# Kernel optimization log

Hardware: AMD Instinct MI355X
Metric: run time of the kernel (lower is better)

## Reference

```python
import jax, jax.numpy as jnp
import numpy as np

FEATURE_DIM = 128
HIDDEN_DIM = 64
MAPPING_SIZE = 64
SCALE = 10.0
B, N, H, W = 8, 65536, 56, 56


def setup_inputs() -> dict:
    key = jax.random.key(0)
    ks = jax.random.split(key, 12)
    features = jax.random.normal(ks[0], (B, FEATURE_DIM, H, W), dtype=jnp.float32)
    # points in [-1, 1]^3
    points = jax.random.uniform(ks[1], (B, N, 3), dtype=jnp.float32, minval=-1.0, maxval=1.0)
    # realistic pinhole intrinsics for a 56x56 feature map
    k_mat = jnp.array([[56.0, 0.0, 28.0], [0.0, 56.0, 28.0], [0.0, 0.0, 1.0]], dtype=jnp.float32)
    k = jnp.broadcast_to(k_mat, (B, 3, 3))
    # extrinsics: identity rotation, translate z by 2 so points are in front of camera
    rt_mat = jnp.concatenate([jnp.eye(3, dtype=jnp.float32), jnp.array([[0.0], [0.0], [2.0]], dtype=jnp.float32)], axis=1)
    rt = jnp.broadcast_to(rt_mat, (B, 3, 4))
    # learned params
    B_gauss = jax.random.normal(ks[2], (MAPPING_SIZE, 3), dtype=jnp.float32) * SCALE
    input_dim = FEATURE_DIM + 2 * MAPPING_SIZE
    W1 = jax.random.normal(ks[3], (input_dim, HIDDEN_DIM), dtype=jnp.float32) * 0.05
    b1 = jnp.zeros((HIDDEN_DIM,), dtype=jnp.float32)
    W2 = jax.random.normal(ks[4], (HIDDEN_DIM, HIDDEN_DIM), dtype=jnp.float32) * 0.05
    b2 = jnp.zeros((HIDDEN_DIM,), dtype=jnp.float32)
    W3 = jax.random.normal(ks[5], (HIDDEN_DIM, HIDDEN_DIM), dtype=jnp.float32) * 0.05
    b3 = jnp.zeros((HIDDEN_DIM,), dtype=jnp.float32)
    W4 = jax.random.normal(ks[6], (HIDDEN_DIM, 1), dtype=jnp.float32) * 0.05
    b4 = jnp.zeros((1,), dtype=jnp.float32)
    return {"features": features, "points": points, "k": k, "rt": rt,
            "B_gauss": B_gauss, "W1": W1, "b1": b1, "W2": W2, "b2": b2,
            "W3": W3, "b3": b3, "W4": W4, "b4": b4}


def _grid_sample_bilinear_zeros(grid, x, y):
    # grid: (B, C, H, W); x, y: (B, N) pixel coords (align_corners=False already unnormalized)
    Bc, C, Hc, Wc = grid.shape
    g = jnp.transpose(grid, (0, 2, 3, 1))  # (B, H, W, C)
    x0 = jnp.floor(x)
    y0 = jnp.floor(y)
    wx1 = x - x0  # frac
    wy1 = y - y0
    wx0 = 1.0 - wx1
    wy0 = 1.0 - wy1
    x0i = x0.astype(jnp.int32)
    y0i = y0.astype(jnp.int32)
    bidx = jnp.arange(Bc, dtype=jnp.int32)[:, None]  # (B, 1)

    def gather(ix, iy):
        inb = ((ix >= 0) & (ix < Wc) & (iy >= 0) & (iy < Hc)).astype(grid.dtype)  # (B, N)
        vals = g[bidx, jnp.clip(iy, 0, Hc - 1), jnp.clip(ix, 0, Wc - 1)]  # (B, N, C)
        return vals * inb[..., None]

    out = (gather(x0i, y0i) * (wx0 * wy0)[..., None]
           + gather(x0i + 1, y0i) * (wx1 * wy0)[..., None]
           + gather(x0i, y0i + 1) * (wx0 * wy1)[..., None]
           + gather(x0i + 1, y0i + 1) * (wx1 * wy1)[..., None])
    return out  # (B, N, C)


def reference(features, points, k, rt, B_gauss, W1, b1, W2, b2, W3, b3, W4, b4):
    Bc, Nc, _ = points.shape
    Hc, Wc = features.shape[-2:]
    # --- camera projection ---
    homo = jnp.concatenate([points, jnp.ones((Bc, Nc, 1), dtype=points.dtype)], axis=2)  # (B,N,4)
    cam = jnp.einsum('bij,bnj->bni', rt, homo)   # (B,N,3)
    img = jnp.einsum('bij,bnj->bni', k, cam)     # (B,N,3)
    z = img[:, :, 2:3] + 1e-8
    uv = img[:, :, :2] / z
    valid = (img[:, :, 2:3] > 0).astype(points.dtype)  # (B,N,1)
    u_norm = (2.0 * uv[..., 0] + 1.0) / Wc - 1.0
    v_norm = (2.0 * uv[..., 1] + 1.0) / Hc - 1.0
    # grid_sample align_corners=False unnormalization: ix = ((g+1)*W - 1)/2
    x = ((u_norm + 1.0) * Wc - 1.0) * 0.5
    y = ((v_norm + 1.0) * Hc - 1.0) * 0.5
    img_feats = _grid_sample_bilinear_zeros(features, x, y) * valid  # (B,N,C)
    # --- Fourier mapping ---
    x_proj = (2.0 * np.pi) * jnp.einsum('bnd,md->bnm', points, B_gauss)  # (B,N,M)
    coord_feats = jnp.concatenate([jnp.sin(x_proj), jnp.cos(x_proj)], axis=-1)  # (B,N,2M)
    # --- MLP ---
    inp = jnp.concatenate([img_feats, coord_feats], axis=2)  # (B,N,C+2M)
    h = jax.nn.relu(inp @ W1 + b1)
    h = jax.nn.relu(h @ W2 + b2)
    h = jax.nn.relu(h @ W3 + b3)
    out = h @ W4 + b4  # (B,N,1)
    return out
```

## Files before the change

kernel.cpp:

```cpp
#include <hip/hip_runtime.h>

#define FDIM 128
#define HDIM 64
#define MSIZE 64
#define IMG_W 56
#define IMG_H 56
#define NPIX (IMG_W * IMG_H)
#define NB 8
#define NPTS 65536

typedef _Float16 f16x8 __attribute__((ext_vector_type(8)));
typedef float f32x4 __attribute__((ext_vector_type(4)));
typedef int i32x4 __attribute__((ext_vector_type(4)));

#define W2_OFF 16384
#define W3_OFF 20480
#define FT_BYTE_OFF 49152
#define TR_BLOCKS (NPIX / 64 * NB)

__device__ __forceinline__ void lds_fence() {
    __asm__ volatile("s_waitcnt lgkmcnt(0)" ::: "memory");
}

__global__ __launch_bounds__(256) void prep_kernel(const float* __restrict__ in,
                                                   const float* __restrict__ W1,
                                                   const float* __restrict__ W2,
                                                   const float* __restrict__ W3,
                                                   _Float16* __restrict__ ws) {
    if (blockIdx.x < TR_BLOCKS) {
        __shared__ float tile[64][129];
        _Float16* out = ws + FT_BYTE_OFF / 2;
        const int b = blockIdx.x / (NPIX / 64);
        const int pbase = (blockIdx.x % (NPIX / 64)) * 64;
        const int t = threadIdx.x;
        const float* src = in + (size_t)b * FDIM * NPIX;
        _Float16*    dst = out + (size_t)b * NPIX * FDIM;
        const int tx = t & 63;
        const int cg = t >> 6;
#pragma unroll
        for (int i = 0; i < 32; ++i) {
            int c = cg * 32 + i;
            tile[tx][c] = src[(size_t)c * NPIX + pbase + tx];
        }
        __syncthreads();
        const int sub = t >> 4;
        const int hk  = (t & 15) * 8;
#pragma unroll
        for (int g = 0; g < 4; ++g) {
            const int px = g * 16 + sub;
            f16x8 hv;
#pragma unroll
            for (int j = 0; j < 8; ++j) hv[j] = (_Float16)tile[px][hk + j];
            *(f16x8*)(dst + (size_t)(pbase + px) * FDIM + hk) = hv;
        }
    } else {
        const int t = (blockIdx.x - TR_BLOCKS) * 256 + threadIdx.x;
        const int l = t & 63;
        const int q = l >> 4;
        const int col = l & 15;
        const int frag = t >> 6;
        if (frag < 32) {
            const int kt = frag >> 2, nt = frag & 3;
#pragma unroll
            for (int j = 0; j < 8; ++j) {
                int k = kt * 32 + q * 8 + j;
                int row = (k < 128) ? k : (128 + (k & 1) * 64 + ((k - 128) >> 1));
                ws[((size_t)(frag * 64 + l)) * 8 + j] = (_Float16)W1[row * HDIM + nt * 16 + col];
            }
        } else if (frag < 40) {
            const int f2 = frag - 32;
            const int kt = f2 >> 2, nt = f2 & 3;
#pragma unroll
            for (int j = 0; j < 8; ++j) {
                int row = kt * 32 + q * 8 + j;
                ws[W2_OFF + ((size_t)(f2 * 64 + l)) * 8 + j] = (_Float16)W2[row * HDIM + nt * 16 + col];
            }
        } else {
            const int f3 = frag - 40;
            const int kt = f3 >> 2, nt = f3 & 3;
#pragma unroll
            for (int j = 0; j < 8; ++j) {
                int row = kt * 32 + q * 8 + j;
                ws[W3_OFF + ((size_t)(f3 * 64 + l)) * 8 + j] = (_Float16)W3[row * HDIM + nt * 16 + col];
            }
        }
    }
}

__global__ __launch_bounds__(256, 2) void decoder_mfma2(
    const _Float16* __restrict__ ft,
    const float* __restrict__ points,
    const float* __restrict__ Kmat, const float* __restrict__ Rt,
    const float* __restrict__ Bg,
    const _Float16* __restrict__ wfrag,
    const float* __restrict__ b1, const float* __restrict__ b2,
    const float* __restrict__ b3,
    const float* __restrict__ W4, const float* __restrict__ b4,
    float* __restrict__ out) {
    __shared__ _Float16 lds[4 * 64 * 72];
    const int tid = threadIdx.x;
    const int wid = tid >> 6;
    const int l   = tid & 63;
    const int q   = l >> 4;
    const int col = l & 15;
    const int b    = blockIdx.x & 7;
    const int grp  = blockIdx.x >> 3;
    const int base = b * NPTS + grp * 256 + wid * 64;
    const int gid  = base + l;
    _Float16* Ah = lds + wid * 64 * 72;
    float* sh = (float*)Ah;
    int*   shi = (int*)Ah;

    const float px = points[(size_t)gid * 3 + 0];
    const float py = points[(size_t)gid * 3 + 1];
    const float pz = points[(size_t)gid * 3 + 2];
    const float* rt = Rt + b * 12;
    const float* km = Kmat + b * 9;
    float cx = rt[0] * px + rt[1] * py + rt[2]  * pz + rt[3];
    float cy = rt[4] * px + rt[5] * py + rt[6]  * pz + rt[7];
    float cz = rt[8] * px + rt[9] * py + rt[10] * pz + rt[11];
    float ix = km[0] * cx + km[1] * cy + km[2] * cz;
    float iy = km[3] * cx + km[4] * cy + km[5] * cz;
    float iz = km[6] * cx + km[7] * cy + km[8] * cz;
    float z  = iz + 1e-8f;
    float u  = ix / z;
    float v  = iy / z;
    float valid = (iz > 0.0f) ? 1.0f : 0.0f;
    float u_norm = (2.0f * u + 1.0f) / (float)IMG_W - 1.0f;
    float v_norm = (2.0f * v + 1.0f) / (float)IMG_H - 1.0f;
    float x = ((u_norm + 1.0f) * (float)IMG_W - 1.0f) * 0.5f;
    float y = ((v_norm + 1.0f) * (float)IMG_H - 1.0f) * 0.5f;
    float x0f = floorf(x), y0f = floorf(y);
    float wx1 = x - x0f, wy1 = y - y0f;
    float wx0 = 1.0f - wx1, wy0 = 1.0f - wy1;
    int x0 = (int)x0f, y0 = (int)y0f;
    int x1 = x0 + 1, y1 = y0 + 1;
    int x0c = x0 < 0 ? 0 : (x0 > IMG_W - 1 ? IMG_W - 1 : x0);
    int x1c = x1 < 0 ? 0 : (x1 > IMG_W - 1 ? IMG_W - 1 : x1);
    int y0c = y0 < 0 ? 0 : (y0 > IMG_H - 1 ? IMG_H - 1 : y0);
    int y1c = y1 < 0 ? 0 : (y1 > IMG_H - 1 ? IMG_H - 1 : y1);
    float mx0 = (x0 >= 0 && x0 < IMG_W) ? 1.0f : 0.0f;
    float mx1 = (x1 >= 0 && x1 < IMG_W) ? 1.0f : 0.0f;
    float my0 = (y0 >= 0 && y0 < IMG_H) ? 1.0f : 0.0f;
    float my1 = (y1 >= 0 && y1 < IMG_H) ? 1.0f : 0.0f;
    const int pb = b * NPIX;
    sh[l * 12 + 0] = wx0 * wy0 * mx0 * my0 * valid;
    sh[l * 12 + 1] = wx1 * wy0 * mx1 * my0 * valid;
    sh[l * 12 + 2] = wx0 * wy1 * mx0 * my1 * valid;
    sh[l * 12 + 3] = wx1 * wy1 * mx1 * my1 * valid;
    shi[l * 12 + 4] = (pb + y0c * IMG_W + x0c) * FDIM;
    shi[l * 12 + 5] = (pb + y0c * IMG_W + x1c) * FDIM;
    shi[l * 12 + 6] = (pb + y1c * IMG_W + x0c) * FDIM;
    shi[l * 12 + 7] = (pb + y1c * IMG_W + x1c) * FDIM;
    sh[l * 12 + 8]  = px;
    sh[l * 12 + 9]  = py;
    sh[l * 12 + 10] = pz;
    lds_fence();

    const f32x4 zero4 = {0.0f, 0.0f, 0.0f, 0.0f};
    f32x4 acc[4][4];
#pragma unroll
    for (int mt = 0; mt < 4; ++mt)
#pragma unroll
        for (int nt = 0; nt < 4; ++nt) acc[mt][nt] = zero4;

    f32x4 wv[4];
    i32x4 iv[4];
    float qx[4], qy[4], qz[4];
#pragma unroll
    for (int mt = 0; mt < 4; ++mt) {
        const float* e = sh + (mt * 16 + col) * 12;
        wv[mt] = *(const f32x4*)(e);
        iv[mt] = *(const i32x4*)(e + 4);
        qx[mt] = e[8]; qy[mt] = e[9]; qz[mt] = e[10];
    }

#pragma unroll
    for (int ktf = 0; ktf < 4; ++ktf) {
        float bgx[4], bgy[4], bgz[4];
#pragma unroll
        for (int i = 0; i < 4; ++i) {
            const int m = ktf * 16 + q * 4 + i;
            bgx[i] = Bg[m * 3 + 0];
            bgy[i] = Bg[m * 3 + 1];
            bgz[i] = Bg[m * 3 + 2];
        }
        f16x8 bf[4];
#pragma unroll
        for (int nt = 0; nt < 4; ++nt)
            bf[nt] = *(const f16x8*)(wfrag + ((size_t)(((4 + ktf) * 4 + nt) * 64 + l)) * 8);
#pragma unroll
        for (int mt = 0; mt < 4; ++mt) {
            f16x8 af;
#pragma unroll
            for (int i = 0; i < 4; ++i) {
                float t = bgx[i] * qx[mt] + bgy[i] * qy[mt] + bgz[i] * qz[mt];
                float tf = t - floorf(t);
                af[2 * i]     = (_Float16)__builtin_amdgcn_sinf(tf);
                af[2 * i + 1] = (_Float16)__builtin_amdgcn_cosf(tf);
            }
#pragma unroll
            for (int nt = 0; nt < 4; ++nt)
                acc[mt][nt] = __builtin_amdgcn_mfma_f32_16x16x32_f16(af, bf[nt], acc[mt][nt], 0, 0, 0);
        }
    }

#pragma unroll
    for (int mt = 0; mt < 4; ++mt) {
        const _Float16 w0h = (_Float16)wv[mt].x, w1h = (_Float16)wv[mt].y;
        const _Float16 w2h = (_Float16)wv[mt].z, w3h = (_Float16)wv[mt].w;
        const int co0 = q * 8;
        f16x8 c00 = *(const f16x8*)(ft + iv[mt].x + co0);
        f16x8 c10 = *(const f16x8*)(ft + iv[mt].y + co0);
        f16x8 c01 = *(const f16x8*)(ft + iv[mt].z + co0);
        f16x8 c11 = *(const f16x8*)(ft + iv[mt].w + co0);
#pragma unroll
        for (int ktg = 0; ktg < 4; ++ktg) {
            f16x8 n00, n10, n01, n11;
            if (ktg < 3) {
                const int co = (ktg + 1) * 32 + q * 8;
                n00 = *(const f16x8*)(ft + iv[mt].x + co);
                n10 = *(const f16x8*)(ft + iv[mt].y + co);
                n01 = *(const f16x8*)(ft + iv[mt].z + co);
                n11 = *(const f16x8*)(ft + iv[mt].w + co);
            }
            f16x8 af = c00 * w0h + c10 * w1h + c01 * w2h + c11 * w3h;
#pragma unroll
            for (int nt = 0; nt < 4; ++nt) {
                f16x8 bf = *(const f16x8*)(wfrag + ((size_t)((ktg * 4 + nt) * 64 + l)) * 8);
                acc[mt][nt] = __builtin_amdgcn_mfma_f32_16x16x32_f16(af, bf, acc[mt][nt], 0, 0, 0);
            }
            c00 = n00; c10 = n10; c01 = n01; c11 = n11;
        }
    }

    float bb[4];
#pragma unroll
    for (int nt = 0; nt < 4; ++nt) bb[nt] = b1[nt * 16 + col];
#pragma unroll
    for (int mt = 0; mt < 4; ++mt)
#pragma unroll
        for (int nt = 0; nt < 4; ++nt)
#pragma unroll
            for (int r = 0; r < 4; ++r) {
                float hv = fmaxf(acc[mt][nt][r] + bb[nt], 0.0f);
                Ah[(mt * 16 + q * 4 + r) * 72 + nt * 16 + col] = (_Float16)hv;
            }
    lds_fence();

#pragma unroll
    for (int mt = 0; mt < 4; ++mt)
#pragma unroll
        for (int nt = 0; nt < 4; ++nt) acc[mt][nt] = zero4;
#pragma unroll
    for (int ktl = 0; ktl < 2; ++ktl) {
        f16x8 bf[4];
#pragma unroll
        for (int nt = 0; nt < 4; ++nt)
            bf[nt] = *(const f16x8*)(wfrag + W2_OFF + ((size_t)((ktl * 4 + nt) * 64 + l)) * 8);
#pragma unroll
        for (int mt = 0; mt < 4; ++mt) {
            f16x8 af = *(const f16x8*)(&Ah[(mt * 16 + col) * 72 + ktl * 32 + q * 8]);
#pragma unroll
            for (int nt = 0; nt < 4; ++nt)
                acc[mt][nt] = __builtin_amdgcn_mfma_f32_16x16x32_f16(af, bf[nt], acc[mt][nt], 0, 0, 0);
        }
    }
    lds_fence();
#pragma unroll
    for (int nt = 0; nt < 4; ++nt) bb[nt] = b2[nt * 16 + col];
#pragma unroll
    for (int mt = 0; mt < 4; ++mt)
#pragma unroll
        for (int nt = 0; nt < 4; ++nt)
#pragma unroll
            for (int r = 0; r < 4; ++r) {
                float hv = fmaxf(acc[mt][nt][r] + bb[nt], 0.0f);
                Ah[(mt * 16 + q * 4 + r) * 72 + nt * 16 + col] = (_Float16)hv;
            }
    lds_fence();

#pragma unroll
    for (int mt = 0; mt < 4; ++mt)
#pragma unroll
        for (int nt = 0; nt < 4; ++nt) acc[mt][nt] = zero4;
#pragma unroll
    for (int ktl = 0; ktl < 2; ++ktl) {
        f16x8 bf[4];
#pragma unroll
        for (int nt = 0; nt < 4; ++nt)
            bf[nt] = *(const f16x8*)(wfrag + W3_OFF + ((size_t)((ktl * 4 + nt) * 64 + l)) * 8);
#pragma unroll
        for (int mt = 0; mt < 4; ++mt) {
            f16x8 af = *(const f16x8*)(&Ah[(mt * 16 + col) * 72 + ktl * 32 + q * 8]);
#pragma unroll
            for (int nt = 0; nt < 4; ++nt)
                acc[mt][nt] = __builtin_amdgcn_mfma_f32_16x16x32_f16(af, bf[nt], acc[mt][nt], 0, 0, 0);
        }
    }

    float b3v[4], w4v[4];
#pragma unroll
    for (int nt = 0; nt < 4; ++nt) {
        b3v[nt] = b3[nt * 16 + col];
        w4v[nt] = W4[nt * 16 + col];
    }
    const float b4v = b4[0];
#pragma unroll
    for (int mt = 0; mt < 4; ++mt)
#pragma unroll
        for (int r = 0; r < 4; ++r) {
            float p = 0.0f;
#pragma unroll
            for (int nt = 0; nt < 4; ++nt)
                p = fmaf(fmaxf(acc[mt][nt][r] + b3v[nt], 0.0f), w4v[nt], p);
            p += __shfl_xor(p, 1);
            p += __shfl_xor(p, 2);
            p += __shfl_xor(p, 4);
            p += __shfl_xor(p, 8);
            if (col == 0) out[base + mt * 16 + q * 4 + r] = p + b4v;
        }
}

__global__ __launch_bounds__(64, 2) void decoder_valu(
    const float* __restrict__ feats, const float* __restrict__ points,
    const float* __restrict__ Kmat, const float* __restrict__ Rt,
    const float* __restrict__ Bg,
    const float* __restrict__ W1, const float* __restrict__ b1,
    const float* __restrict__ W2, const float* __restrict__ b2,
    const float* __restrict__ W3, const float* __restrict__ b3,
    const float* __restrict__ W4, const float* __restrict__ b4,
    float* __restrict__ out) {
    __shared__ float hbuf[64 * 65];
    const int tid = threadIdx.x;
    const int b   = blockIdx.x / (NPTS / 64);
    const int gid = blockIdx.x * 64 + tid;
    const float px = points[(size_t)gid * 3 + 0];
    const float py = points[(size_t)gid * 3 + 1];
    const float pz = points[(size_t)gid * 3 + 2];
    const float* rt = Rt + b * 12;
    const float* km = Kmat + b * 9;
    float cx = rt[0] * px + rt[1] * py + rt[2]  * pz + rt[3];
    float cy = rt[4] * px + rt[5] * py + rt[6]  * pz + rt[7];
    float cz = rt[8] * px + rt[9] * py + rt[10] * pz + rt[11];
    float ix = km[0] * cx + km[1] * cy + km[2] * cz;
    float iy = km[3] * cx + km[4] * cy + km[5] * cz;
    float iz = km[6] * cx + km[7] * cy + km[8] * cz;
    float z  = iz + 1e-8f;
    float u  = ix / z, v = iy / z;
    float valid = (iz > 0.0f) ? 1.0f : 0.0f;
    float u_norm = (2.0f * u + 1.0f) / (float)IMG_W - 1.0f;
    float v_norm = (2.0f * v + 1.0f) / (float)IMG_H - 1.0f;
    float x = ((u_norm + 1.0f) * (float)IMG_W - 1.0f) * 0.5f;
    float y = ((v_norm + 1.0f) * (float)IMG_H - 1.0f) * 0.5f;
    float x0f = floorf(x), y0f = floorf(y);
    float wx1 = x - x0f, wy1 = y - y0f;
    float wx0 = 1.0f - wx1, wy0 = 1.0f - wy1;
    int x0 = (int)x0f, y0 = (int)y0f;
    int x1 = x0 + 1, y1 = y0 + 1;
    int x0c = x0 < 0 ? 0 : (x0 > IMG_W - 1 ? IMG_W - 1 : x0);
    int x1c = x1 < 0 ? 0 : (x1 > IMG_W - 1 ? IMG_W - 1 : x1);
    int y0c = y0 < 0 ? 0 : (y0 > IMG_H - 1 ? IMG_H - 1 : y0);
    int y1c = y1 < 0 ? 0 : (y1 > IMG_H - 1 ? IMG_H - 1 : y1);
    float mx0 = (x0 >= 0 && x0 < IMG_W) ? 1.0f : 0.0f;
    float mx1 = (x1 >= 0 && x1 < IMG_W) ? 1.0f : 0.0f;
    float my0 = (y0 >= 0 && y0 < IMG_H) ? 1.0f : 0.0f;
    float my1 = (y1 >= 0 && y1 < IMG_H) ? 1.0f : 0.0f;
    float w00 = wx0 * wy0 * mx0 * my0 * valid;
    float w10 = wx1 * wy0 * mx1 * my0 * valid;
    float w01 = wx0 * wy1 * mx0 * my1 * valid;
    float w11 = wx1 * wy1 * mx1 * my1 * valid;
    float h[HDIM];
#pragma unroll
    for (int j = 0; j < HDIM; ++j) h[j] = b1[j];
    const float* fb = feats + (size_t)b * FDIM * NPIX;
    const int p00 = y0c * IMG_W + x0c, p10 = y0c * IMG_W + x1c;
    const int p01 = y1c * IMG_W + x0c, p11 = y1c * IMG_W + x1c;
#pragma unroll 1
    for (int c = 0; c < FDIM; ++c) {
        const float* fp = fb + (size_t)c * NPIX;
        float fv = w00 * fp[p00] + w10 * fp[p10] + w01 * fp[p01] + w11 * fp[p11];
        const float* wr = W1 + (size_t)c * HDIM;
#pragma unroll
        for (int j = 0; j < HDIM; ++j) h[j] = fmaf(fv, wr[j], h[j]);
    }
#pragma unroll 1
    for (int m = 0; m < MSIZE; ++m) {
        float t = Bg[m * 3 + 0] * px + Bg[m * 3 + 1] * py + Bg[m * 3 + 2] * pz;
        float tf = t - floorf(t);
        float s = __builtin_amdgcn_sinf(tf);
        float c = __builtin_amdgcn_cosf(tf);
        const float* wsn = W1 + (size_t)(FDIM + m) * HDIM;
        const float* wcs = W1 + (size_t)(FDIM + MSIZE + m) * HDIM;
#pragma unroll
        for (int j = 0; j < HDIM; ++j)
            h[j] = fmaf(s, wsn[j], fmaf(c, wcs[j], h[j]));
    }
    float* myh = &hbuf[tid * 65];
#pragma unroll
    for (int j = 0; j < HDIM; ++j) myh[j] = fmaxf(h[j], 0.0f);
    float h2[HDIM];
#pragma unroll
    for (int j = 0; j < HDIM; ++j) h2[j] = b2[j];
#pragma unroll 1
    for (int i = 0; i < HDIM; ++i) {
        float hi = myh[i];
        const float* wr = W2 + (size_t)i * HDIM;
#pragma unroll
        for (int j = 0; j < HDIM; ++j) h2[j] = fmaf(hi, wr[j], h2[j]);
    }
#pragma unroll
    for (int j = 0; j < HDIM; ++j) myh[j] = fmaxf(h2[j], 0.0f);
#pragma unroll
    for (int j = 0; j < HDIM; ++j) h[j] = b3[j];
#pragma unroll 1
    for (int i = 0; i < HDIM; ++i) {
        float hi = myh[i];
        const float* wr = W3 + (size_t)i * HDIM;
#pragma unroll
        for (int j = 0; j < HDIM; ++j) h[j] = fmaf(hi, wr[j], h[j]);
    }
    float acc = b4[0];
#pragma unroll
    for (int j = 0; j < HDIM; ++j) acc = fmaf(fmaxf(h[j], 0.0f), W4[j], acc);
    out[gid] = acc;
}

extern "C" void kernel_launch(void* const* d_in, const int* in_sizes, int n_in,
                              void* d_out, int out_size, void* d_ws, size_t ws_size,
                              hipStream_t stream) {
    const float* feats = (const float*)d_in[0];
    const float* pts   = (const float*)d_in[1];
    const float* k     = (const float*)d_in[2];
    const float* rt    = (const float*)d_in[3];
    const float* Bg    = (const float*)d_in[4];
    const float* W1    = (const float*)d_in[5];
    const float* b1    = (const float*)d_in[6];
    const float* W2    = (const float*)d_in[7];
    const float* b2    = (const float*)d_in[8];
    const float* W3    = (const float*)d_in[9];
    const float* b3    = (const float*)d_in[10];
    const float* W4    = (const float*)d_in[11];
    const float* b4    = (const float*)d_in[12];
    float* out = (float*)d_out;

    const size_t ftBytes = (size_t)NB * NPIX * FDIM * sizeof(_Float16);

    if (ws_size >= FT_BYTE_OFF + ftBytes) {
        _Float16* wf = (_Float16*)d_ws;
        _Float16* ft = (_Float16*)((char*)d_ws + FT_BYTE_OFF);
        prep_kernel<<<TR_BLOCKS + 12, 256, 0, stream>>>(feats, W1, W2, W3, wf);
        decoder_mfma2<<<NB * NPTS / 256, 256, 0, stream>>>(ft, pts, k, rt, Bg, wf,
                                                           b1, b2, b3, W4, b4, out);
    } else {
        decoder_valu<<<NB * NPTS / 64, 64, 0, stream>>>(feats, pts, k, rt, Bg,
                                                        W1, b1, W2, b2, W3, b3, W4, b4, out);
    }
}
```

Before: 184.1 us.

## Halve per-wave point tile to raise occupancy and pipeline feature gathers across tiles

The main decoder now handles 32 points per wave (two M-tiles) instead of 64. This roughly halves accumulator registers and LDS per block, and launch bounds allow 4 blocks per CU instead of 2. The gather prefetch now runs across both M-tiles as one flat 8-step pipeline, with the first gather issued before the Fourier phase so its latency overlaps that phase. The transpose prep kernel is reworked to use 16-pixel tiles with float4 loads and packed fp16 conversion, and the Fourier path uses fract/cvt_pkrtz intrinsics. In exchange, weight fragments are reloaded for twice as many waves, and half the lanes sit idle during the projection setup.

```diff
diff --git a/kernel.cpp b/kernel.cpp
--- a/kernel.cpp
+++ b/kernel.cpp
@@ -10,13 +10,14 @@
 #define NPTS 65536
 
 typedef _Float16 f16x8 __attribute__((ext_vector_type(8)));
+typedef __fp16 hf16x2 __attribute__((ext_vector_type(2)));
 typedef float f32x4 __attribute__((ext_vector_type(4)));
 typedef int i32x4 __attribute__((ext_vector_type(4)));
 
 #define W2_OFF 16384
 #define W3_OFF 20480
 #define FT_BYTE_OFF 49152
-#define TR_BLOCKS (NPIX / 64 * NB)
+#define TR16_BLOCKS (NPIX / 16 * NB)
 
 __device__ __forceinline__ void lds_fence() {
     __asm__ volatile("s_waitcnt lgkmcnt(0)" ::: "memory");
@@ -27,34 +28,35 @@
                                                    const float* __restrict__ W2,
                                                    const float* __restrict__ W3,
                                                    _Float16* __restrict__ ws) {
-    if (blockIdx.x < TR_BLOCKS) {
-        __shared__ float tile[64][129];
+    if (blockIdx.x < TR16_BLOCKS) {
+        __shared__ float tile[16][133];
         _Float16* out = ws + FT_BYTE_OFF / 2;
-        const int b = blockIdx.x / (NPIX / 64);
-        const int pbase = (blockIdx.x % (NPIX / 64)) * 64;
+        const int b = blockIdx.x / (NPIX / 16);
+        const int pbase = (blockIdx.x % (NPIX / 16)) * 16;
         const int t = threadIdx.x;
         const float* src = in + (size_t)b * FDIM * NPIX;
         _Float16*    dst = out + (size_t)b * NPIX * FDIM;
-        const int tx = t & 63;
-        const int cg = t >> 6;
-#pragma unroll
-        for (int i = 0; i < 32; ++i) {
-            int c = cg * 32 + i;
-            tile[tx][c] = src[(size_t)c * NPIX + pbase + tx];
+        const int pq = t & 3;
+        const int ch = t >> 2;
+#pragma unroll
+        for (int it = 0; it < 2; ++it) {
+            const int c = it * 64 + ch;
+            const float4 v = *(const float4*)(src + (size_t)c * NPIX + pbase + pq * 4);
+            tile[pq * 4 + 0][c] = v.x;
+            tile[pq * 4 + 1][c] = v.y;
+            tile[pq * 4 + 2][c] = v.z;
+            tile[pq * 4 + 3][c] = v.w;
         }
         __syncthreads();
-        const int sub = t >> 4;
-        const int hk  = (t & 15) * 8;
-#pragma unroll
-        for (int g = 0; g < 4; ++g) {
-            const int px = g * 16 + sub;
-            f16x8 hv;
-#pragma unroll
-            for (int j = 0; j < 8; ++j) hv[j] = (_Float16)tile[px][hk + j];
-            *(f16x8*)(dst + (size_t)(pbase + px) * FDIM + hk) = hv;
-        }
+        const int px = t >> 4;
+        const int hk = (t & 15) * 8;
+        union { f16x8 v; hf16x2 h[4]; } hv;
+#pragma unroll
+        for (int j = 0; j < 4; ++j)
+            hv.h[j] = __builtin_amdgcn_cvt_pkrtz(tile[px][hk + 2 * j], tile[px][hk + 2 * j + 1]);
+        *(f16x8*)(dst + (size_t)(pbase + px) * FDIM + hk) = hv.v;
     } else {
-        const int t = (blockIdx.x - TR_BLOCKS) * 256 + threadIdx.x;
+        const int t = (blockIdx.x - TR16_BLOCKS) * 256 + threadIdx.x;
         const int l = t & 63;
         const int q = l >> 4;
         const int col = l & 15;
@@ -87,7 +89,7 @@
     }
 }
 
-__global__ __launch_bounds__(256, 2) void decoder_mfma2(
+__global__ __launch_bounds__(256, 4) void decoder_mfma3(
     const _Float16* __restrict__ ft,
     const float* __restrict__ points,
     const float* __restrict__ Kmat, const float* __restrict__ Rt,
@@ -97,7 +99,7 @@
     const float* __restrict__ b3,
     const float* __restrict__ W4, const float* __restrict__ b4,
     float* __restrict__ out) {
-    __shared__ _Float16 lds[4 * 64 * 72];
+    __shared__ _Float16 lds[4 * 32 * 72];
     const int tid = threadIdx.x;
     const int wid = tid >> 6;
     const int l   = tid & 63;
@@ -105,75 +107,82 @@
     const int col = l & 15;
     const int b    = blockIdx.x & 7;
     const int grp  = blockIdx.x >> 3;
-    const int base = b * NPTS + grp * 256 + wid * 64;
-    const int gid  = base + l;
-    _Float16* Ah = lds + wid * 64 * 72;
+    const int base = b * NPTS + grp * 128 + wid * 32;
+    _Float16* Ah = lds + wid * 32 * 72;
     float* sh = (float*)Ah;
     int*   shi = (int*)Ah;
 
-    const float px = points[(size_t)gid * 3 + 0];
-    const float py = points[(size_t)gid * 3 + 1];
-    const float pz = points[(size_t)gid * 3 + 2];
-    const float* rt = Rt + b * 12;
-    const float* km = Kmat + b * 9;
-    float cx = rt[0] * px + rt[1] * py + rt[2]  * pz + rt[3];
-    float cy = rt[4] * px + rt[5] * py + rt[6]  * pz + rt[7];
-    float cz = rt[8] * px + rt[9] * py + rt[10] * pz + rt[11];
-    float ix = km[0] * cx + km[1] * cy + km[2] * cz;
-    float iy = km[3] * cx + km[4] * cy + km[5] * cz;
-    float iz = km[6] * cx + km[7] * cy + km[8] * cz;
-    float z  = iz + 1e-8f;
-    float u  = ix / z;
-    float v  = iy / z;
-    float valid = (iz > 0.0f) ? 1.0f : 0.0f;
-    float u_norm = (2.0f * u + 1.0f) / (float)IMG_W - 1.0f;
-    float v_norm = (2.0f * v + 1.0f) / (float)IMG_H - 1.0f;
-    float x = ((u_norm + 1.0f) * (float)IMG_W - 1.0f) * 0.5f;
-    float y = ((v_norm + 1.0f) * (float)IMG_H - 1.0f) * 0.5f;
-    float x0f = floorf(x), y0f = floorf(y);
-    float wx1 = x - x0f, wy1 = y - y0f;
-    float wx0 = 1.0f - wx1, wy0 = 1.0f - wy1;
-    int x0 = (int)x0f, y0 = (int)y0f;
-    int x1 = x0 + 1, y1 = y0 + 1;
-    int x0c = x0 < 0 ? 0 : (x0 > IMG_W - 1 ? IMG_W - 1 : x0);
-    int x1c = x1 < 0 ? 0 : (x1 > IMG_W - 1 ? IMG_W - 1 : x1);
-    int y0c = y0 < 0 ? 0 : (y0 > IMG_H - 1 ? IMG_H - 1 : y0);
-    int y1c = y1 < 0 ? 0 : (y1 > IMG_H - 1 ? IMG_H - 1 : y1);
-    float mx0 = (x0 >= 0 && x0 < IMG_W) ? 1.0f : 0.0f;
-    float mx1 = (x1 >= 0 && x1 < IMG_W) ? 1.0f : 0.0f;
-    float my0 = (y0 >= 0 && y0 < IMG_H) ? 1.0f : 0.0f;
-    float my1 = (y1 >= 0 && y1 < IMG_H) ? 1.0f : 0.0f;
-    const int pb = b * NPIX;
-    sh[l * 12 + 0] = wx0 * wy0 * mx0 * my0 * valid;
-    sh[l * 12 + 1] = wx1 * wy0 * mx1 * my0 * valid;
-    sh[l * 12 + 2] = wx0 * wy1 * mx0 * my1 * valid;
-    sh[l * 12 + 3] = wx1 * wy1 * mx1 * my1 * valid;
-    shi[l * 12 + 4] = (pb + y0c * IMG_W + x0c) * FDIM;
-    shi[l * 12 + 5] = (pb + y0c * IMG_W + x1c) * FDIM;
-    shi[l * 12 + 6] = (pb + y1c * IMG_W + x0c) * FDIM;
-    shi[l * 12 + 7] = (pb + y1c * IMG_W + x1c) * FDIM;
-    sh[l * 12 + 8]  = px;
-    sh[l * 12 + 9]  = py;
-    sh[l * 12 + 10] = pz;
+    if (l < 32) {
+        const int gid = base + l;
+        const float px = points[(size_t)gid * 3 + 0];
+        const float py = points[(size_t)gid * 3 + 1];
+        const float pz = points[(size_t)gid * 3 + 2];
+        const float* rt = Rt + b * 12;
+        const float* km = Kmat + b * 9;
+        float cx = rt[0] * px + rt[1] * py + rt[2]  * pz + rt[3];
+        float cy = rt[4] * px + rt[5] * py + rt[6]  * pz + rt[7];
+        float cz = rt[8] * px + rt[9] * py + rt[10] * pz + rt[11];
+        float ix = km[0] * cx + km[1] * cy + km[2] * cz;
+        float iy = km[3] * cx + km[4] * cy + km[5] * cz;
+        float iz = km[6] * cx + km[7] * cy + km[8] * cz;
+        float z  = iz + 1e-8f;
+        float u  = ix / z;
+        float v  = iy / z;
+        float valid = (iz > 0.0f) ? 1.0f : 0.0f;
+        float u_norm = (2.0f * u + 1.0f) / (float)IMG_W - 1.0f;
+        float v_norm = (2.0f * v + 1.0f) / (float)IMG_H - 1.0f;
+        float x = ((u_norm + 1.0f) * (float)IMG_W - 1.0f) * 0.5f;
+        float y = ((v_norm + 1.0f) * (float)IMG_H - 1.0f) * 0.5f;
+        float x0f = floorf(x), y0f = floorf(y);
+        float wx1 = x - x0f, wy1 = y - y0f;
+        float wx0 = 1.0f - wx1, wy0 = 1.0f - wy1;
+        int x0 = (int)x0f, y0 = (int)y0f;
+        int x1 = x0 + 1, y1 = y0 + 1;
+        int x0c = x0 < 0 ? 0 : (x0 > IMG_W - 1 ? IMG_W - 1 : x0);
+        int x1c = x1 < 0 ? 0 : (x1 > IMG_W - 1 ? IMG_W - 1 : x1);
+        int y0c = y0 < 0 ? 0 : (y0 > IMG_H - 1 ? IMG_H - 1 : y0);
+        int y1c = y1 < 0 ? 0 : (y1 > IMG_H - 1 ? IMG_H - 1 : y1);
+        float mx0 = (x0 >= 0 && x0 < IMG_W) ? 1.0f : 0.0f;
+        float mx1 = (x1 >= 0 && x1 < IMG_W) ? 1.0f : 0.0f;
+        float my0 = (y0 >= 0 && y0 < IMG_H) ? 1.0f : 0.0f;
+        float my1 = (y1 >= 0 && y1 < IMG_H) ? 1.0f : 0.0f;
+        const int pb = b * NPIX;
+        sh[l * 12 + 0] = wx0 * wy0 * mx0 * my0 * valid;
+        sh[l * 12 + 1] = wx1 * wy0 * mx1 * my0 * valid;
+        sh[l * 12 + 2] = wx0 * wy1 * mx0 * my1 * valid;
+        sh[l * 12 + 3] = wx1 * wy1 * mx1 * my1 * valid;
+        shi[l * 12 + 4] = (pb + y0c * IMG_W + x0c) * FDIM;
+        shi[l * 12 + 5] = (pb + y0c * IMG_W + x1c) * FDIM;
+        shi[l * 12 + 6] = (pb + y1c * IMG_W + x0c) * FDIM;
+        shi[l * 12 + 7] = (pb + y1c * IMG_W + x1c) * FDIM;
+        sh[l * 12 + 8]  = px;
+        sh[l * 12 + 9]  = py;
+        sh[l * 12 + 10] = pz;
+    }
     lds_fence();
 
     const f32x4 zero4 = {0.0f, 0.0f, 0.0f, 0.0f};
-    f32x4 acc[4][4];
-#pragma unroll
-    for (int mt = 0; mt < 4; ++mt)
+    f32x4 acc[2][4];
+#pragma unroll
+    for (int mt = 0; mt < 2; ++mt)
 #pragma unroll
         for (int nt = 0; nt < 4; ++nt) acc[mt][nt] = zero4;
 
-    f32x4 wv[4];
-    i32x4 iv[4];
-    float qx[4], qy[4], qz[4];
-#pragma unroll
-    for (int mt = 0; mt < 4; ++mt) {
+    f32x4 wv[2];
+    i32x4 iv[2];
+    float qx[2], qy[2], qz[2];
+#pragma unroll
+    for (int mt = 0; mt < 2; ++mt) {
         const float* e = sh + (mt * 16 + col) * 12;
         wv[mt] = *(const f32x4*)(e);
         iv[mt] = *(const i32x4*)(e + 4);
         qx[mt] = e[8]; qy[mt] = e[9]; qz[mt] = e[10];
     }
+
+    f16x8 c00 = *(const f16x8*)(ft + iv[0].x + q * 8);
+    f16x8 c10 = *(const f16x8*)(ft + iv[0].y + q * 8);
+    f16x8 c01 = *(const f16x8*)(ft + iv[0].z + q * 8);
+    f16x8 c11 = *(const f16x8*)(ft + iv[0].w + q * 8);
 
 #pragma unroll
     for (int ktf = 0; ktf < 4; ++ktf) {
@@ -190,55 +199,53 @@
         for (int nt = 0; nt < 4; ++nt)
             bf[nt] = *(const f16x8*)(wfrag + ((size_t)(((4 + ktf) * 4 + nt) * 64 + l)) * 8);
 #pragma unroll
-        for (int mt = 0; mt < 4; ++mt) {
-            f16x8 af;
+        for (int mt = 0; mt < 2; ++mt) {
+            union { f16x8 v; hf16x2 h[4]; } af;
 #pragma unroll
             for (int i = 0; i < 4; ++i) {
                 float t = bgx[i] * qx[mt] + bgy[i] * qy[mt] + bgz[i] * qz[mt];
-                float tf = t - floorf(t);
-                af[2 * i]     = (_Float16)__builtin_amdgcn_sinf(tf);
-                af[2 * i + 1] = (_Float16)__builtin_amdgcn_cosf(tf);
+                float tf = __builtin_amdgcn_fractf(t);
+                af.h[i] = __builtin_amdgcn_cvt_pkrtz(__builtin_amdgcn_sinf(tf),
+                                                     __builtin_amdgcn_cosf(tf));
             }
 #pragma unroll
             for (int nt = 0; nt < 4; ++nt)
-                acc[mt][nt] = __builtin_amdgcn_mfma_f32_16x16x32_f16(af, bf[nt], acc[mt][nt], 0, 0, 0);
-        }
-    }
-
-#pragma unroll
-    for (int mt = 0; mt < 4; ++mt) {
-        const _Float16 w0h = (_Float16)wv[mt].x, w1h = (_Float16)wv[mt].y;
-        const _Float16 w2h = (_Float16)wv[mt].z, w3h = (_Float16)wv[mt].w;
-        const int co0 = q * 8;
-        f16x8 c00 = *(const f16x8*)(ft + iv[mt].x + co0);
-        f16x8 c10 = *(const f16x8*)(ft + iv[mt].y + co0);
-        f16x8 c01 = *(const f16x8*)(ft + iv[mt].z + co0);
-        f16x8 c11 = *(const f16x8*)(ft + iv[mt].w + co0);
-#pragma unroll
-        for (int ktg = 0; ktg < 4; ++ktg) {
-            f16x8 n00, n10, n01, n11;
-            if (ktg < 3) {
-                const int co = (ktg + 1) * 32 + q * 8;
-                n00 = *(const f16x8*)(ft + iv[mt].x + co);
-                n10 = *(const f16x8*)(ft + iv[mt].y + co);
-                n01 = *(const f16x8*)(ft + iv[mt].z + co);
-                n11 = *(const f16x8*)(ft + iv[mt].w + co);
-            }
-            f16x8 af = c00 * w0h + c10 * w1h + c01 * w2h + c11 * w3h;
-#pragma unroll
-            for (int nt = 0; nt < 4; ++nt) {
-                f16x8 bf = *(const f16x8*)(wfrag + ((size_t)((ktg * 4 + nt) * 64 + l)) * 8);
-                acc[mt][nt] = __builtin_amdgcn_mfma_f32_16x16x32_f16(af, bf, acc[mt][nt], 0, 0, 0);
-            }
-            c00 = n00; c10 = n10; c01 = n01; c11 = n11;
-        }
+                acc[mt][nt] = __builtin_amdgcn_mfma_f32_16x16x32_f16(af.v, bf[nt], acc[mt][nt], 0, 0, 0);
+        }
+    }
+
+    _Float16 wh[2][4];
+#pragma unroll
+    for (int mt = 0; mt < 2; ++mt) {
+        wh[mt][0] = (_Float16)wv[mt].x; wh[mt][1] = (_Float16)wv[mt].y;
+        wh[mt][2] = (_Float16)wv[mt].z; wh[mt][3] = (_Float16)wv[mt].w;
+    }
+#pragma unroll
+    for (int s = 0; s < 8; ++s) {
+        const int mt = s >> 2, ktg = s & 3;
+        f16x8 n00, n10, n01, n11;
+        if (s < 7) {
+            const int nmt = (s + 1) >> 2, nktg = (s + 1) & 3;
+            const int co = nktg * 32 + q * 8;
+            n00 = *(const f16x8*)(ft + iv[nmt].x + co);
+            n10 = *(const f16x8*)(ft + iv[nmt].y + co);
+            n01 = *(const f16x8*)(ft + iv[nmt].z + co);
+            n11 = *(const f16x8*)(ft + iv[nmt].w + co);
+        }
+        f16x8 af = c00 * wh[mt][0] + c10 * wh[mt][1] + c01 * wh[mt][2] + c11 * wh[mt][3];
+#pragma unroll
+        for (int nt = 0; nt < 4; ++nt) {
+            f16x8 bf = *(const f16x8*)(wfrag + ((size_t)((ktg * 4 + nt) * 64 + l)) * 8);
+            acc[mt][nt] = __builtin_amdgcn_mfma_f32_16x16x32_f16(af, bf, acc[mt][nt], 0, 0, 0);
+        }
+        c00 = n00; c10 = n10; c01 = n01; c11 = n11;
     }
 
     float bb[4];
 #pragma unroll
     for (int nt = 0; nt < 4; ++nt) bb[nt] = b1[nt * 16 + col];
 #pragma unroll
-    for (int mt = 0; mt < 4; ++mt)
+    for (int mt = 0; mt < 2; ++mt)
 #pragma unroll
         for (int nt = 0; nt < 4; ++nt)
 #pragma unroll
@@ -249,7 +256,7 @@
     lds_fence();
 
 #pragma unroll
-    for (int mt = 0; mt < 4; ++mt)
+    for (int mt = 0; mt < 2; ++mt)
 #pragma unroll
         for (int nt = 0; nt < 4; ++nt) acc[mt][nt] = zero4;
 #pragma unroll
@@ -259,7 +266,7 @@
         for (int nt = 0; nt < 4; ++nt)
             bf[nt] = *(const f16x8*)(wfrag + W2_OFF + ((size_t)((ktl * 4 + nt) * 64 + l)) * 8);
 #pragma unroll
-        for (int mt = 0; mt < 4; ++mt) {
+        for (int mt = 0; mt < 2; ++mt) {
             f16x8 af = *(const f16x8*)(&Ah[(mt * 16 + col) * 72 + ktl * 32 + q * 8]);
 #pragma unroll
             for (int nt = 0; nt < 4; ++nt)
@@ -270,7 +277,7 @@
 #pragma unroll
     for (int nt = 0; nt < 4; ++nt) bb[nt] = b2[nt * 16 + col];
 #pragma unroll
-    for (int mt = 0; mt < 4; ++mt)
+    for (int mt = 0; mt < 2; ++mt)
 #pragma unroll
         for (int nt = 0; nt < 4; ++nt)
 #pragma unroll
@@ -281,7 +288,7 @@
     lds_fence();
 
 #pragma unroll
-    for (int mt = 0; mt < 4; ++mt)
+    for (int mt = 0; mt < 2; ++mt)
 #pragma unroll
         for (int nt = 0; nt < 4; ++nt) acc[mt][nt] = zero4;
 #pragma unroll
@@ -291,7 +298,7 @@
         for (int nt = 0; nt < 4; ++nt)
             bf[nt] = *(const f16x8*)(wfrag + W3_OFF + ((size_t)((ktl * 4 + nt) * 64 + l)) * 8);
 #pragma unroll
-        for (int mt = 0; mt < 4; ++mt) {
+        for (int mt = 0; mt < 2; ++mt) {
             f16x8 af = *(const f16x8*)(&Ah[(mt * 16 + col) * 72 + ktl * 32 + q * 8]);
 #pragma unroll
             for (int nt = 0; nt < 4; ++nt)
@@ -307,7 +314,7 @@
     }
     const float b4v = b4[0];
 #pragma unroll
-    for (int mt = 0; mt < 4; ++mt)
+    for (int mt = 0; mt < 2; ++mt)
 #pragma unroll
         for (int r = 0; r < 4; ++r) {
             float p = 0.0f;
@@ -449,8 +456,8 @@
     if (ws_size >= FT_BYTE_OFF + ftBytes) {
         _Float16* wf = (_Float16*)d_ws;
         _Float16* ft = (_Float16*)((char*)d_ws + FT_BYTE_OFF);
-        prep_kernel<<<TR_BLOCKS + 12, 256, 0, stream>>>(feats, W1, W2, W3, wf);
-        decoder_mfma2<<<NB * NPTS / 256, 256, 0, stream>>>(ft, pts, k, rt, Bg, wf,
+        prep_kernel<<<TR16_BLOCKS + 12, 256, 0, stream>>>(feats, W1, W2, W3, wf);
+        decoder_mfma3<<<NB * NPTS / 128, 256, 0, stream>>>(ft, pts, k, rt, Bg, wf,
                                                            b1, b2, b3, W4, b4, out);
     } else {
         decoder_valu<<<NB * NPTS / 64, 64, 0, stream>>>(feats, pts, k, rt, Bg,
```

New measurement: 182.3 us. About the same (-1.0%).
